# Performance work log

Hardware: AMD Instinct MI355X
Metric: run time of the kernel (lower is better)

The kernel has to match this reference:

```python
import jax, jax.numpy as jnp
import numpy as np

# bin sizes: logspace(-3,0,20) seconds, keep those < (t_end - t_start)/2 = 0.25 s, in ms
_bs = np.logspace(-3, 0, 20)
BIN_MS = [int(b) for b in np.round(_bs[_bs < 0.25] * 1000).astype(int)]  # 16 bins: [1,1,2,3,4,6,9,13,18,26,38,55,78,113,162,234]

SYNC_COST = 10.0
T_START_MS, T_END_MS = 0, 500
EPS = 1e-7


def setup_inputs() -> dict:
    C, B, T, N, N_E = 50, 8, 600, 30000, 24000
    rng = np.random.default_rng(42)
    spikes = (rng.random((B, T, N)) < 0.02).astype(np.float32)
    sample_trials = rng.integers(0, B, size=C).astype(np.int32)
    # sample_counts ~ N(70, 30) clipped to [15, N_E], consecutive chunks of a shuffled e-id list
    counts = np.clip(rng.normal(70.0, 30.0, C).astype(np.int64), 15, N_E)
    e_ids = rng.permutation(N_E)
    sel_mask = np.zeros((C, N), dtype=bool)
    prev = 0
    for i in range(C):
        cn = int(counts[i])
        if prev + cn > N_E:
            e_ids = rng.permutation(e_ids)
            prev = 0
        sel_mask[i, e_ids[prev:prev + cn]] = True
        prev += cn
    exp_fanos = (rng.random(len(BIN_MS)) * 1.5 + 0.5).astype(np.float32)
    return {
        "spikes": jnp.asarray(spikes),
        "exp_fanos": jnp.asarray(exp_fanos),
        "sample_trials": jnp.asarray(sample_trials),
        "sel_mask": jnp.asarray(sel_mask),
    }


def reference(spikes, exp_fanos, sample_trials, sel_mask):
    # trim to analysis window: [B, 500, N]
    sp = spikes[:, T_START_MS:T_END_MS, :]
    C = sel_mask.shape[0]
    m = sel_mask.astype(sp.dtype)  # [C, N]
    # population spike count per sample: sum over selected e-cells.
    # M[b, t, c] = sum_n sp[b,t,n] * m[c,n]; then pick the sampled trial per c.
    M = jnp.einsum('btn,cn->btc', sp, m)                 # [B, T, C] (small)
    selected = M[sample_trials, :, jnp.arange(C)]        # [C, T]
    T = selected.shape[1]
    fanos = []
    for b in BIN_MS:  # fixed small set of bin sizes
        nb = T // b
        # conv1d(ones, stride=b, VALID) == non-overlapping binned sums
        counts = selected[:, :nb * b].reshape(C, nb, b).sum(axis=-1)  # [C, nb]
        mean_count = jnp.maximum(counts.mean(axis=1), EPS)
        var_count = counts.var(axis=1)  # population variance, matches tf.math.reduce_variance
        fanos.append(jnp.mean(var_count / mean_count))
    fanos = jnp.stack(fanos)  # [16]
    mse_loss = jnp.mean(jnp.square(exp_fanos - fanos))
    return SYNC_COST * mse_loss
```

## Files before the change

### kernel.cpp

```cpp
#include <hip/hip_runtime.h>

#define C_CLS 50
#define B_TR 8
#define T_FULL 600
#define T_USE 500
#define N_NEU 30000
#define NGRP 118
#define NGRP_PAD 120
#define WPC 480
#define NQUAD 30
#define NBINS 16
#define EPS 1e-7
#define LDS_STRIDE 501

__device__ __constant__ int d_bins[NBINS] = {1,1,2,3,4,6,9,13,18,26,38,55,78,113,162,234};


__global__ void init_tc_kernel(const int* __restrict__ trials, int* flags,
                               int* ncls, int* cls_of_trial) {
    int lane = threadIdx.x;
    if (lane < 8) flags[lane] = 0;
    int b = (lane < C_CLS) ? trials[lane] : -1;
    for (int bb = 0; bb < B_TR; ++bb) {
        unsigned long long m = __ballot(b == bb);
        if (b == bb) {
            int pos = __popcll(m & ((1ull << lane) - 1ull));
            cls_of_trial[bb * 64 + pos] = lane;
        }
        if (lane == 0) ncls[bb] = __popcll(m);
    }
}

__global__ void detect_mode_kernel(const unsigned int* __restrict__ w, int* flags) {
    const int nwords = C_CLS * N_NEU / 4;
    int stride = gridDim.x * blockDim.x;
    int fF = 0, fB = 0, fO = 0, fD = 0;
    for (int i = blockIdx.x * blockDim.x + threadIdx.x; i < nwords; i += stride) {
        unsigned int v = w[i];
        if (v == 0u) continue;
        if (v == 0x3F800000u) fF = 1;
        else if (v == 0x3FF00000u && (i & 1)) fD = 1;
        else {
            unsigned int b0 = v & 0xFFu, b1 = (v >> 8) & 0xFFu,
                         b2 = (v >> 16) & 0xFFu, b3 = (v >> 24) & 0xFFu;
            bool byteOK = (b0 <= 1u) && (b1 <= 1u) && (b2 <= 1u) && (b3 <= 1u);
            if (byteOK && v != 1u) fB = 1;
        }
        if (i & 1) fO = 1;
    }
    if (fF) atomicOr(&flags[0], 1);
    if (fB) atomicOr(&flags[1], 1);
    if (fO) atomicOr(&flags[2], 1);
    if (fD) atomicOr(&flags[3], 1);
}

__device__ __forceinline__ int mode_from_flags(const int* flags) {
    if (flags[0]) return 2;
    if (flags[3]) return 4;
    if (flags[1]) return 1;
    if (flags[2]) return 0;
    return 3;
}

__device__ __forceinline__ bool load_sel(const void* mask, int mode, long long e) {
    switch (mode) {
        case 0:  return ((const int*)mask)[e] != 0;
        case 1:  return ((const unsigned char*)mask)[e] != 0;
        case 2:  return ((const float*)mask)[e] != 0.0f;
        case 3:  return ((const long long*)mask)[e] != 0LL;
        default: return ((const double*)mask)[e] != 0.0;
    }
}

__global__ void build_bits_kernel(const void* mask, const int* flags,
                                  unsigned long long* bits) {
    int c = blockIdx.x;
    int lane = threadIdx.x;
    int mode = mode_from_flags(flags);
    for (int g = blockIdx.y; g < NGRP_PAD; g += gridDim.y) {
        int base = g * 256 + lane * 4;
        long long e = (long long)c * N_NEU + base;
        bool s0 = (base + 0 < N_NEU) && load_sel(mask, mode, e + 0);
        bool s1 = (base + 1 < N_NEU) && load_sel(mask, mode, e + 1);
        bool s2 = (base + 2 < N_NEU) && load_sel(mask, mode, e + 2);
        bool s3 = (base + 3 < N_NEU) && load_sel(mask, mode, e + 3);
        unsigned long long w0 = __ballot(s0);
        unsigned long long w1 = __ballot(s1);
        unsigned long long w2 = __ballot(s2);
        unsigned long long w3 = __ballot(s3);
        if (lane == 0) {
            long long o = (long long)c * WPC + g * 4;
            bits[o + 0] = w0; bits[o + 1] = w1;
            bits[o + 2] = w2; bits[o + 3] = w3;
        }
    }
}

__global__ void __launch_bounds__(256)
stream_kernel(const float* __restrict__ spikes,
              const int* __restrict__ ncls,
              const int* __restrict__ cls_of_trial,
              const unsigned long long* __restrict__ bits,
              float* __restrict__ selected) {
    int bt = blockIdx.x;
    int b = bt / T_USE;
    int t = bt - b * T_USE;
    int nc = ncls[b];
    if (nc == 0) return;
    int lane = threadIdx.x & 63;
    int wid = threadIdx.x >> 6;
    int myc = cls_of_trial[b * 64 + (lane < nc ? lane : 0)];
    const ulonglong2* __restrict__ bp2 = (const ulonglong2*)bits;
    long long base2 = (long long)myc * (WPC / 2);
    const float4* __restrict__ row4 =
        (const float4*)(spikes + ((long long)b * T_FULL + t) * N_NEU);
    int q0 = (wid * 15) >> 1;
    int q1 = ((wid + 1) * 15) >> 1;
    int acc = 0;
    for (int q = q0; q < q1; ++q) {
        int gbase = q * 4;
        float4 v[4];
        ulonglong2 w[8];
#pragma unroll
        for (int u = 0; u < 4; ++u) {
            int ia = (gbase + u) * 64 + lane;
            if (ia > N_NEU / 4 - 1) ia = N_NEU / 4 - 1;
            v[u] = row4[ia];
        }
#pragma unroll
        for (int u = 0; u < 8; ++u) w[u] = bp2[base2 + q * 8 + u];
#pragma unroll
        for (int u = 0; u < 4; ++u) {
            unsigned long long b0 = __ballot(v[u].x != 0.0f);
            unsigned long long b1 = __ballot(v[u].y != 0.0f);
            unsigned long long b2 = __ballot(v[u].z != 0.0f);
            unsigned long long b3 = __ballot(v[u].w != 0.0f);
            acc += __popcll(b0 & w[2 * u].x) + __popcll(b1 & w[2 * u].y)
                 + __popcll(b2 & w[2 * u + 1].x) + __popcll(b3 & w[2 * u + 1].y);
        }
    }
    __shared__ int sacc[4][64];
    sacc[wid][lane] = acc;
    __syncthreads();
    if (wid == 0 && lane < nc) {
        int s = sacc[0][lane] + sacc[1][lane] + sacc[2][lane] + sacc[3][lane];
        selected[myc * T_USE + t] = (float)s;
    }
}

__global__ void __launch_bounds__(1024)
fano_loss_kernel(const float* __restrict__ selected,
                 const float* __restrict__ exp_fanos,
                 float* __restrict__ out) {
    __shared__ float lds[C_CLS * LDS_STRIDE];
    __shared__ float sf[NBINS];
    const float4* __restrict__ sel4 = (const float4*)selected;
    for (int i = threadIdx.x; i < C_CLS * T_USE / 4; i += 1024) {
        float4 v = sel4[i];
        int r = i / (T_USE / 4);
        int p = (i - r * (T_USE / 4)) * 4;
        float* dst = &lds[r * LDS_STRIDE + p];
        dst[0] = v.x; dst[1] = v.y; dst[2] = v.z; dst[3] = v.w;
    }
    __syncthreads();
    int wid = threadIdx.x >> 6;
    int lane = threadIdx.x & 63;
    int b = d_bins[wid];
    int nb = T_USE / b;
    float fano = 0.f;
    if (lane < C_CLS) {
        const float* row = &lds[lane * LDS_STRIDE];
        double s1 = 0.0, s2 = 0.0;
        for (int i = 0; i < nb; ++i) {
            float cs = 0.f;
            int base = i * b;
            for (int j = 0; j < b; ++j) cs += row[base + j];
            s1 += cs;
            s2 += (double)cs * (double)cs;
        }
        double mean = s1 / nb;
        double var = s2 / nb - mean * mean;
        if (var < 0.0) var = 0.0;
        double m = mean > EPS ? mean : EPS;
        fano = (float)(var / m);
    }
    for (int off = 32; off > 0; off >>= 1) fano += __shfl_down(fano, off);
    if (lane == 0) sf[wid] = fano / (float)C_CLS;
    __syncthreads();
    if (wid == 0) {
        float sq = 0.f;
        if (lane < NBINS) {
            float d = exp_fanos[lane] - sf[lane];
            sq = d * d;
        }
        for (int off = 32; off > 0; off >>= 1) sq += __shfl_down(sq, off);
        if (lane == 0) out[0] = 10.0f * sq / (float)NBINS;
    }
}

extern "C" void kernel_launch(void* const* d_in, const int* in_sizes, int n_in,
                              void* d_out, int out_size, void* d_ws, size_t ws_size,
                              hipStream_t stream) {
    const float* spikes    = (const float*)d_in[0];
    const float* exp_fanos = (const float*)d_in[1];
    const int*   trials    = (const int*)d_in[2];
    const void*  mask      = d_in[3];
    float* out = (float*)d_out;

    char* ws = (char*)d_ws;
    int*   flags   = (int*)(ws + 0);
    int*   ncls    = (int*)(ws + 256);
    int*   clsofb  = (int*)(ws + 512);
    unsigned long long* bits = (unsigned long long*)(ws + 8192);
    float* selected = (float*)(ws + 204800);

    init_tc_kernel<<<1, 64, 0, stream>>>(trials, flags, ncls, clsofb);
    detect_mode_kernel<<<256, 256, 0, stream>>>((const unsigned int*)mask, flags);
    build_bits_kernel<<<dim3(C_CLS, 8), 64, 0, stream>>>(mask, flags, bits);
    stream_kernel<<<B_TR * T_USE, 256, 0, stream>>>(spikes, ncls, clsofb, bits, selected);
    fano_loss_kernel<<<1, 1024, 0, stream>>>(selected, exp_fanos, out);
}
```

Measured before the change: 184.0 us.

## Build per-row spike bitmask in LDS and popcount against class masks cooperatively

The stream kernel now ballots each spike row into a shared-memory bitmask first. It then loops over the classes mapped to that trial, and all 256 threads popcount coalesced words of each class mask, with wave-shuffle and LDS reductions. Before, every lane reloaded its own class's full 480-word mask, so mask traffic per block scaled with 64 lanes. The cost is an extra barrier plus one shuffle reduction per class, serialized over the classes of the trial.

```diff
diff --git a/kernel.cpp b/kernel.cpp
--- a/kernel.cpp
+++ b/kernel.cpp
@@ -7,8 +7,8 @@
 #define N_NEU 30000
 #define NGRP 118
 #define NGRP_PAD 120
+#define NWORDS 472
 #define WPC 480
-#define NQUAD 30
 #define NBINS 16
 #define EPS 1e-7
 #define LDS_STRIDE 501
@@ -102,6 +102,8 @@
               const int* __restrict__ cls_of_trial,
               const unsigned long long* __restrict__ bits,
               float* __restrict__ selected) {
+    __shared__ unsigned long long sbits[NWORDS];
+    __shared__ int wsum[52][4];
     int bt = blockIdx.x;
     int b = bt / T_USE;
     int t = bt - b * T_USE;
@@ -109,42 +111,67 @@
     if (nc == 0) return;
     int lane = threadIdx.x & 63;
     int wid = threadIdx.x >> 6;
-    int myc = cls_of_trial[b * 64 + (lane < nc ? lane : 0)];
-    const ulonglong2* __restrict__ bp2 = (const ulonglong2*)bits;
-    long long base2 = (long long)myc * (WPC / 2);
     const float4* __restrict__ row4 =
         (const float4*)(spikes + ((long long)b * T_FULL + t) * N_NEU);
-    int q0 = (wid * 15) >> 1;
-    int q1 = ((wid + 1) * 15) >> 1;
-    int acc = 0;
-    for (int q = q0; q < q1; ++q) {
-        int gbase = q * 4;
+
+    int g0 = wid * 30;
+    int g1 = g0 + 30; if (g1 > NGRP) g1 = NGRP;
+    int g = g0;
+    for (; g + 4 <= g1; g += 4) {
         float4 v[4];
-        ulonglong2 w[8];
 #pragma unroll
         for (int u = 0; u < 4; ++u) {
-            int ia = (gbase + u) * 64 + lane;
+            int ia = (g + u) * 64 + lane;
             if (ia > N_NEU / 4 - 1) ia = N_NEU / 4 - 1;
             v[u] = row4[ia];
         }
-#pragma unroll
-        for (int u = 0; u < 8; ++u) w[u] = bp2[base2 + q * 8 + u];
 #pragma unroll
         for (int u = 0; u < 4; ++u) {
             unsigned long long b0 = __ballot(v[u].x != 0.0f);
             unsigned long long b1 = __ballot(v[u].y != 0.0f);
             unsigned long long b2 = __ballot(v[u].z != 0.0f);
             unsigned long long b3 = __ballot(v[u].w != 0.0f);
-            acc += __popcll(b0 & w[2 * u].x) + __popcll(b1 & w[2 * u].y)
-                 + __popcll(b2 & w[2 * u + 1].x) + __popcll(b3 & w[2 * u + 1].y);
-        }
-    }
-    __shared__ int sacc[4][64];
-    sacc[wid][lane] = acc;
-    __syncthreads();
-    if (wid == 0 && lane < nc) {
-        int s = sacc[0][lane] + sacc[1][lane] + sacc[2][lane] + sacc[3][lane];
-        selected[myc * T_USE + t] = (float)s;
+            if (lane == 0) {
+                int o = (g + u) * 4;
+                sbits[o + 0] = b0; sbits[o + 1] = b1;
+                sbits[o + 2] = b2; sbits[o + 3] = b3;
+            }
+        }
+    }
+    for (; g < g1; ++g) {
+        int ia = g * 64 + lane;
+        if (ia > N_NEU / 4 - 1) ia = N_NEU / 4 - 1;
+        float4 v = row4[ia];
+        unsigned long long b0 = __ballot(v.x != 0.0f);
+        unsigned long long b1 = __ballot(v.y != 0.0f);
+        unsigned long long b2 = __ballot(v.z != 0.0f);
+        unsigned long long b3 = __ballot(v.w != 0.0f);
+        if (lane == 0) {
+            int o = g * 4;
+            sbits[o + 0] = b0; sbits[o + 1] = b1;
+            sbits[o + 2] = b2; sbits[o + 3] = b3;
+        }
+    }
+    __syncthreads();
+
+    int i0 = threadIdx.x;
+    int i1 = threadIdx.x + 256;
+    unsigned long long s0 = sbits[i0];
+    unsigned long long s1 = (i1 < NWORDS) ? sbits[i1] : 0ull;
+    for (int kc = 0; kc < nc; ++kc) {
+        int c = cls_of_trial[b * 64 + kc];
+        const unsigned long long* __restrict__ bp = bits + (long long)c * WPC;
+        int p = __popcll(s0 & bp[i0]);
+        if (i1 < NWORDS) p += __popcll(s1 & bp[i1]);
+        for (int off = 32; off > 0; off >>= 1) p += __shfl_down(p, off);
+        if (lane == 0) wsum[kc][wid] = p;
+    }
+    __syncthreads();
+    if (threadIdx.x < nc) {
+        int c = cls_of_trial[b * 64 + threadIdx.x];
+        int s = wsum[threadIdx.x][0] + wsum[threadIdx.x][1]
+              + wsum[threadIdx.x][2] + wsum[threadIdx.x][3];
+        selected[c * T_USE + t] = (float)s;
     }
 }
 
```

Result: no change. 184.5 us (+0.3%).

## Process four timesteps per block and merge init with mask detection

Applied to the files above, without the earlier changes.

The streaming kernel now gives each wave one timestep row, with four timesteps per block. It stores the spike ballot bitmasks in LDS, then loops over the classes of that trial. For each class it loads the class bit-words once and reuses them across the four timesteps, using packed 16-bit partial sums and shuffle reductions. The old per-lane class layout, which reloaded mask words for every timestep, is gone. The trial/class init kernel is folded into the mask-detection kernel, which now writes per-block verdicts, removing one launch and the need to zero the flags. The cost is serial per-class reduction loops and extra LDS traffic.

```diff
diff --git a/kernel.cpp b/kernel.cpp
--- a/kernel.cpp
+++ b/kernel.cpp
@@ -8,7 +8,8 @@
 #define NGRP 118
 #define NGRP_PAD 120
 #define WPC 480
-#define NQUAD 30
+#define NQ 30
+#define TPB 4
 #define NBINS 16
 #define EPS 1e-7
 #define LDS_STRIDE 501
@@ -16,49 +17,11 @@
 __device__ __constant__ int d_bins[NBINS] = {1,1,2,3,4,6,9,13,18,26,38,55,78,113,162,234};
 
 
-__global__ void init_tc_kernel(const int* __restrict__ trials, int* flags,
-                               int* ncls, int* cls_of_trial) {
-    int lane = threadIdx.x;
-    if (lane < 8) flags[lane] = 0;
-    int b = (lane < C_CLS) ? trials[lane] : -1;
-    for (int bb = 0; bb < B_TR; ++bb) {
-        unsigned long long m = __ballot(b == bb);
-        if (b == bb) {
-            int pos = __popcll(m & ((1ull << lane) - 1ull));
-            cls_of_trial[bb * 64 + pos] = lane;
-        }
-        if (lane == 0) ncls[bb] = __popcll(m);
-    }
-}
-
-__global__ void detect_mode_kernel(const unsigned int* __restrict__ w, int* flags) {
-    const int nwords = C_CLS * N_NEU / 4;
-    int stride = gridDim.x * blockDim.x;
-    int fF = 0, fB = 0, fO = 0, fD = 0;
-    for (int i = blockIdx.x * blockDim.x + threadIdx.x; i < nwords; i += stride) {
-        unsigned int v = w[i];
-        if (v == 0u) continue;
-        if (v == 0x3F800000u) fF = 1;
-        else if (v == 0x3FF00000u && (i & 1)) fD = 1;
-        else {
-            unsigned int b0 = v & 0xFFu, b1 = (v >> 8) & 0xFFu,
-                         b2 = (v >> 16) & 0xFFu, b3 = (v >> 24) & 0xFFu;
-            bool byteOK = (b0 <= 1u) && (b1 <= 1u) && (b2 <= 1u) && (b3 <= 1u);
-            if (byteOK && v != 1u) fB = 1;
-        }
-        if (i & 1) fO = 1;
-    }
-    if (fF) atomicOr(&flags[0], 1);
-    if (fB) atomicOr(&flags[1], 1);
-    if (fO) atomicOr(&flags[2], 1);
-    if (fD) atomicOr(&flags[3], 1);
-}
-
-__device__ __forceinline__ int mode_from_flags(const int* flags) {
-    if (flags[0]) return 2;
-    if (flags[3]) return 4;
-    if (flags[1]) return 1;
-    if (flags[2]) return 0;
+__device__ __forceinline__ int mode_from_verdict(int v) {
+    if (v & 1) return 2;
+    if (v & 8) return 4;
+    if (v & 2) return 1;
+    if (v & 4) return 0;
     return 3;
 }
 
@@ -72,11 +35,55 @@
     }
 }
 
-__global__ void build_bits_kernel(const void* mask, const int* flags,
+__global__ void __launch_bounds__(256)
+detect_kernel(const unsigned int* __restrict__ w, const int* __restrict__ trials,
+              int* verdict, int* ncls, int* cls_of_trial) {
+    __shared__ int sfl;
+    if (threadIdx.x == 0) sfl = 0;
+    __syncthreads();
+    const int nwords = C_CLS * N_NEU / 4;
+    int per = (nwords + gridDim.x - 1) / gridDim.x;
+    int beg = blockIdx.x * per;
+    int end = beg + per; if (end > nwords) end = nwords;
+    int f = 0;
+    for (int i = beg + threadIdx.x; i < end; i += blockDim.x) {
+        unsigned int v = w[i];
+        if (v == 0u) continue;
+        if (v == 0x3F800000u) f |= 1;
+        else if (v == 0x3FF00000u && (i & 1)) f |= 8;
+        else {
+            unsigned int b0 = v & 0xFFu, b1 = (v >> 8) & 0xFFu,
+                         b2 = (v >> 16) & 0xFFu, b3 = (v >> 24) & 0xFFu;
+            bool byteOK = (b0 <= 1u) && (b1 <= 1u) && (b2 <= 1u) && (b3 <= 1u);
+            if (byteOK && v != 1u) f |= 2;
+        }
+        if (i & 1) f |= 4;
+    }
+    if (f) atomicOr(&sfl, f);
+    __syncthreads();
+    if (threadIdx.x == 0) verdict[blockIdx.x] = sfl;
+
+    if (blockIdx.x == 0 && threadIdx.x < 64) {
+        int lane = threadIdx.x;
+        int b = (lane < C_CLS) ? trials[lane] : -1;
+        for (int bb = 0; bb < B_TR; ++bb) {
+            unsigned long long m = __ballot(b == bb);
+            if (b == bb) {
+                int pos = __popcll(m & ((1ull << lane) - 1ull));
+                cls_of_trial[bb * 64 + pos] = lane;
+            }
+            if (lane == 0) ncls[bb] = __popcll(m);
+        }
+    }
+}
+
+__global__ void build_bits_kernel(const void* mask, const int* __restrict__ verdict,
                                   unsigned long long* bits) {
     int c = blockIdx.x;
     int lane = threadIdx.x;
-    int mode = mode_from_flags(flags);
+    int v = verdict[lane] | verdict[lane + 64] | verdict[lane + 128] | verdict[lane + 192];
+    for (int off = 32; off > 0; off >>= 1) v |= __shfl_xor(v, off);
+    int mode = mode_from_verdict(v);
     for (int g = blockIdx.y; g < NGRP_PAD; g += gridDim.y) {
         int base = g * 256 + lane * 4;
         long long e = (long long)c * N_NEU + base;
@@ -102,49 +109,78 @@
               const int* __restrict__ cls_of_trial,
               const unsigned long long* __restrict__ bits,
               float* __restrict__ selected) {
+    __shared__ unsigned long long sbits[TPB][WPC];
+    __shared__ int wsum2[C_CLS][4][2];
     int bt = blockIdx.x;
-    int b = bt / T_USE;
-    int t = bt - b * T_USE;
+    int b = bt / (T_USE / TPB);
+    int tq = bt - b * (T_USE / TPB);
+    int t0 = tq * TPB;
     int nc = ncls[b];
     if (nc == 0) return;
     int lane = threadIdx.x & 63;
     int wid = threadIdx.x >> 6;
-    int myc = cls_of_trial[b * 64 + (lane < nc ? lane : 0)];
-    const ulonglong2* __restrict__ bp2 = (const ulonglong2*)bits;
-    long long base2 = (long long)myc * (WPC / 2);
     const float4* __restrict__ row4 =
-        (const float4*)(spikes + ((long long)b * T_FULL + t) * N_NEU);
-    int q0 = (wid * 15) >> 1;
-    int q1 = ((wid + 1) * 15) >> 1;
-    int acc = 0;
-    for (int q = q0; q < q1; ++q) {
-        int gbase = q * 4;
+        (const float4*)(spikes + ((long long)(b * T_FULL + t0 + wid)) * N_NEU);
+
+    for (int q = 0; q < NQ; ++q) {
         float4 v[4];
-        ulonglong2 w[8];
 #pragma unroll
         for (int u = 0; u < 4; ++u) {
-            int ia = (gbase + u) * 64 + lane;
+            int ia = (q * 4 + u) * 64 + lane;
             if (ia > N_NEU / 4 - 1) ia = N_NEU / 4 - 1;
             v[u] = row4[ia];
         }
-#pragma unroll
-        for (int u = 0; u < 8; ++u) w[u] = bp2[base2 + q * 8 + u];
 #pragma unroll
         for (int u = 0; u < 4; ++u) {
             unsigned long long b0 = __ballot(v[u].x != 0.0f);
             unsigned long long b1 = __ballot(v[u].y != 0.0f);
             unsigned long long b2 = __ballot(v[u].z != 0.0f);
             unsigned long long b3 = __ballot(v[u].w != 0.0f);
-            acc += __popcll(b0 & w[2 * u].x) + __popcll(b1 & w[2 * u].y)
-                 + __popcll(b2 & w[2 * u + 1].x) + __popcll(b3 & w[2 * u + 1].y);
-        }
-    }
-    __shared__ int sacc[4][64];
-    sacc[wid][lane] = acc;
-    __syncthreads();
-    if (wid == 0 && lane < nc) {
-        int s = sacc[0][lane] + sacc[1][lane] + sacc[2][lane] + sacc[3][lane];
-        selected[myc * T_USE + t] = (float)s;
+            if (lane == 0) {
+                int o = (q * 4 + u) * 4;
+                sbits[wid][o + 0] = b0; sbits[wid][o + 1] = b1;
+                sbits[wid][o + 2] = b2; sbits[wid][o + 3] = b3;
+            }
+        }
+    }
+    __syncthreads();
+
+    int i0 = threadIdx.x;
+    int i1 = threadIdx.x + 256;
+    bool has1 = (i1 < WPC);
+    unsigned long long s00 = sbits[0][i0], s10 = sbits[1][i0],
+                       s20 = sbits[2][i0], s30 = sbits[3][i0];
+    unsigned long long s01 = 0, s11 = 0, s21 = 0, s31 = 0;
+    if (has1) { s01 = sbits[0][i1]; s11 = sbits[1][i1];
+                s21 = sbits[2][i1]; s31 = sbits[3][i1]; }
+    for (int kc = 0; kc < nc; ++kc) {
+        int c = cls_of_trial[b * 64 + kc];
+        const unsigned long long* __restrict__ bp = bits + (long long)c * WPC;
+        unsigned long long w0 = bp[i0];
+        unsigned long long w1 = has1 ? bp[i1] : 0ull;
+        int p0 = __popcll(s00 & w0) + __popcll(s01 & w1);
+        int p1 = __popcll(s10 & w0) + __popcll(s11 & w1);
+        int p2 = __popcll(s20 & w0) + __popcll(s21 & w1);
+        int p3 = __popcll(s30 & w0) + __popcll(s31 & w1);
+        int pa = p0 | (p1 << 16);
+        int pb = p2 | (p3 << 16);
+        for (int off = 32; off > 0; off >>= 1) {
+            pa += __shfl_down(pa, off);
+            pb += __shfl_down(pb, off);
+        }
+        if (lane == 0) { wsum2[kc][wid][0] = pa; wsum2[kc][wid][1] = pb; }
+    }
+    __syncthreads();
+    if (threadIdx.x < nc * 4) {
+        int kc = threadIdx.x >> 2, r = threadIdx.x & 3;
+        int c = cls_of_trial[b * 64 + kc];
+        int s = 0;
+#pragma unroll
+        for (int w = 0; w < 4; ++w) {
+            int v = wsum2[kc][w][r >> 1];
+            s += (r & 1) ? (v >> 16) : (v & 0xFFFF);
+        }
+        selected[c * T_USE + t0 + r] = (float)s;
     }
 }
 
@@ -208,15 +244,16 @@
     float* out = (float*)d_out;
 
     char* ws = (char*)d_ws;
-    int*   flags   = (int*)(ws + 0);
-    int*   ncls    = (int*)(ws + 256);
-    int*   clsofb  = (int*)(ws + 512);
+    int*   verdict = (int*)(ws + 0);
+    int*   ncls    = (int*)(ws + 1024);
+    int*   clsofb  = (int*)(ws + 1280);
     unsigned long long* bits = (unsigned long long*)(ws + 8192);
     float* selected = (float*)(ws + 204800);
 
-    init_tc_kernel<<<1, 64, 0, stream>>>(trials, flags, ncls, clsofb);
-    detect_mode_kernel<<<256, 256, 0, stream>>>((const unsigned int*)mask, flags);
-    build_bits_kernel<<<dim3(C_CLS, 8), 64, 0, stream>>>(mask, flags, bits);
-    stream_kernel<<<B_TR * T_USE, 256, 0, stream>>>(spikes, ncls, clsofb, bits, selected);
+    detect_kernel<<<256, 256, 0, stream>>>((const unsigned int*)mask, trials,
+                                           verdict, ncls, clsofb);
+    build_bits_kernel<<<dim3(C_CLS, 8), 64, 0, stream>>>(mask, verdict, bits);
+    stream_kernel<<<B_TR * (T_USE / TPB), 256, 0, stream>>>(spikes, ncls, clsofb,
+                                                            bits, selected);
     fano_loss_kernel<<<1, 1024, 0, stream>>>(selected, exp_fanos, out);
 }
```

Result: no change. 181.3 us (-1.5%).
